# Performance work log

Hardware: AMD Instinct MI355X
Metric: run time of the kernel (lower is better)

## Reference

```python
import jax, jax.numpy as jnp
import numpy as np

B, D, ADA, INTER, RANK = 16, 2048, 1024, 1024, 8

def setup_inputs() -> dict:
    key = jax.random.key(0)
    ks = jax.random.split(key, 7)
    s = lambda fan_in: 1.0 / np.sqrt(fan_in)
    return {
        "x": jax.random.normal(ks[0], (B, D), jnp.float32),
        "ada_emb": jax.random.normal(ks[1], (B, ADA), jnp.float32),
        "base": jax.random.normal(ks[2], (D, D), jnp.float32),  # nn.Parameter(torch.randn)
        "w1": jax.random.normal(ks[3], (ADA, INTER), jnp.float32) * s(ADA),
        "b1": jax.random.normal(ks[4], (INTER,), jnp.float32) * s(ADA),
        "w2": jax.random.normal(ks[5], (INTER, D * RANK * 2), jnp.float32) * s(INTER),
        "b2": jax.random.normal(ks[6], (D * RANK * 2,), jnp.float32) * s(INTER),
    }

def reference(x, ada_emb, base, w1, b1, w2, b2):
    Bn, Dn = x.shape
    # gen_weight: Linear -> GELU (exact, erf-based as torch nn.GELU) -> Linear
    h = jax.nn.gelu(ada_emb @ w1 + b1, approximate=False)
    xw = h @ w2 + b2                               # [B, D*rank*2]
    x_a, x_b = jnp.split(xw, 2, axis=-1)
    r = x_a.shape[-1] // Dn
    x_a = x_a.reshape(Bn, Dn, r)                   # [B, D, r]
    x_b = x_b.reshape(Bn, Dn, r)                   # [B, D, r]
    # per-sample low-rank delta + base: layer[b,d,k] = base[d,k] + sum_r x_a[b,d,r]*x_b[b,k,r]
    layer = base[None, :, :] + jnp.einsum('bdr,bkr->bdk', x_a, x_b)  # [B, D, D]
    out = jnp.einsum('bc,bco->bo', x, layer)       # batched matvec
    return x + out                                 # residual
```

## Files before the change

kernel.cpp:

```cpp
#include <hip/hip_runtime.h>
#include <math.h>

#define BN 16
#define DN 2048
#define ADA 1024
#define INTER 1024
#define NW2 32768
#define HALFN 16384

__global__ void k1a(const float* __restrict__ ada, const float* __restrict__ w1,
                    float* __restrict__ h_pre) {
    const int j  = blockIdx.x * 256 + threadIdx.x;
    const int k0 = blockIdx.y * 32;
    __shared__ float a_lds[BN][32];
    for (int idx = threadIdx.x; idx < BN * 32; idx += 256) {
        int m = idx >> 5, kk = idx & 31;
        a_lds[m][kk] = ada[m * ADA + k0 + kk];
    }
    __syncthreads();
    float acc[BN];
#pragma unroll
    for (int m = 0; m < BN; ++m) acc[m] = 0.f;
    for (int kk = 0; kk < 32; ++kk) {
        float w = w1[(k0 + kk) * INTER + j];
#pragma unroll
        for (int m = 0; m < BN; ++m) acc[m] += a_lds[m][kk] * w;
    }
#pragma unroll
    for (int m = 0; m < BN; ++m) atomicAdd(&h_pre[m * INTER + j], acc[m]);
}

__global__ void k1bt(const float* __restrict__ h_pre, const float* __restrict__ b1,
                     float* __restrict__ h_t) {
    int i = blockIdx.x * 256 + threadIdx.x;
    int m = i >> 10, j = i & (INTER - 1);
    float v = h_pre[i] + b1[j];
    float g = 0.5f * v * (1.f + erff(v * 0.70710678118654752f));
    h_t[j * BN + m] = g;
}

#define K2ACC(i, hv) do { acc[i].x = fmaf((hv), w.x, acc[i].x); \
                          acc[i].y = fmaf((hv), w.y, acc[i].y); } while (0)
__global__ __launch_bounds__(256) void k2m(const float* __restrict__ h_t,
                                           const float* __restrict__ w2,
                                           float* __restrict__ p2) {
    const int n2 = blockIdx.x * 256 + threadIdx.x;
    const int k0 = blockIdx.y * 128;
    float2 acc[BN];
#pragma unroll
    for (int m = 0; m < BN; ++m) acc[m] = make_float2(0.f, 0.f);

    const float2* wp = (const float2*)w2 + (size_t)k0 * (NW2 / 2) + n2;
    const float4* hp = (const float4*)h_t + (size_t)k0 * 4;

    float2 wbuf[8];
#pragma unroll
    for (int u = 0; u < 8; ++u) wbuf[u] = wp[(size_t)u * (NW2 / 2)];

    for (int kb = 0; kb < 128; kb += 8) {
#pragma unroll
        for (int u = 0; u < 8; ++u) {
            const int k = kb + u;
            const float2 w = wbuf[u];
            const int kn = (k + 8 < 128) ? (k + 8) : k;
            wbuf[u] = wp[(size_t)kn * (NW2 / 2)];
            const float4 h0 = hp[k * 4 + 0];
            const float4 h1 = hp[k * 4 + 1];
            const float4 h2 = hp[k * 4 + 2];
            const float4 h3 = hp[k * 4 + 3];
            K2ACC(0,  h0.x); K2ACC(1,  h0.y); K2ACC(2,  h0.z); K2ACC(3,  h0.w);
            K2ACC(4,  h1.x); K2ACC(5,  h1.y); K2ACC(6,  h1.z); K2ACC(7,  h1.w);
            K2ACC(8,  h2.x); K2ACC(9,  h2.y); K2ACC(10, h2.z); K2ACC(11, h2.w);
            K2ACC(12, h3.x); K2ACC(13, h3.y); K2ACC(14, h3.z); K2ACC(15, h3.w);
        }
    }
    float2* op = (float2*)p2 + (size_t)blockIdx.y * (BN * NW2 / 2) + n2;
#pragma unroll
    for (int m = 0; m < BN; ++m) op[(size_t)m * (NW2 / 2)] = acc[m];
}

__global__ void k2r(const float* __restrict__ p2, const float* __restrict__ b2,
                    float* __restrict__ xw) {
    const int i  = blockIdx.x * 256 + threadIdx.x;
    const int n4 = i & (NW2 / 4 - 1);
    float4 s = ((const float4*)b2)[n4];
    const float4* p = (const float4*)p2 + i;
#pragma unroll
    for (int ks = 0; ks < 8; ++ks) {
        float4 v = p[(size_t)ks * (BN * NW2 / 4)];
        s.x += v.x; s.y += v.y; s.z += v.z; s.w += v.w;
    }
    ((float4*)xw)[i] = s;
}

__global__ void k3(const float* __restrict__ x, const float* __restrict__ xw,
                   float* __restrict__ t) {
    const int m = blockIdx.x >> 3, r = blockIdx.x & 7;
    float s = 0.f;
    for (int c = threadIdx.x; c < DN; c += 256)
        s += x[m * DN + c] * xw[(size_t)m * NW2 + c * 8 + r];
    __shared__ float red[256];
    red[threadIdx.x] = s;
    __syncthreads();
    for (int off = 128; off > 0; off >>= 1) {
        if (threadIdx.x < off) red[threadIdx.x] += red[threadIdx.x + off];
        __syncthreads();
    }
    if (threadIdx.x == 0) t[m * 8 + r] = red[0];
}

#define K4ACC(i, xv) do { acc[i].x = fmaf((xv), b.x, acc[i].x); \
                          acc[i].y = fmaf((xv), b.y, acc[i].y); \
                          acc[i].z = fmaf((xv), b.z, acc[i].z); \
                          acc[i].w = fmaf((xv), b.w, acc[i].w); } while (0)
__global__ __launch_bounds__(256) void k4m(const float* __restrict__ x,
                                           const float* __restrict__ base,
                                           float* __restrict__ p4) {
    const int o4 = blockIdx.x * 256 + threadIdx.x;
    const int c0 = blockIdx.y * 32;
    const int m0 = blockIdx.z * 8;
    float4 acc[8];
#pragma unroll
    for (int m = 0; m < 8; ++m) acc[m] = make_float4(0.f, 0.f, 0.f, 0.f);

    const float4* bp = (const float4*)base + (size_t)c0 * (DN / 4) + o4;
    float4 bbuf[8];
#pragma unroll
    for (int u = 0; u < 8; ++u) bbuf[u] = bp[(size_t)u * (DN / 4)];

    for (int cb = 0; cb < 32; cb += 8) {
#pragma unroll
        for (int u = 0; u < 8; ++u) {
            const int cc = cb + u;
            const float4 b = bbuf[u];
            const int cn = (cc + 8 < 32) ? (cc + 8) : cc;
            bbuf[u] = bp[(size_t)cn * (DN / 4)];
            const float x0 = x[(m0 + 0) * DN + c0 + cc];
            const float x1 = x[(m0 + 1) * DN + c0 + cc];
            const float x2 = x[(m0 + 2) * DN + c0 + cc];
            const float x3 = x[(m0 + 3) * DN + c0 + cc];
            const float x4 = x[(m0 + 4) * DN + c0 + cc];
            const float x5 = x[(m0 + 5) * DN + c0 + cc];
            const float x6 = x[(m0 + 6) * DN + c0 + cc];
            const float x7 = x[(m0 + 7) * DN + c0 + cc];
            K4ACC(0, x0); K4ACC(1, x1); K4ACC(2, x2); K4ACC(3, x3);
            K4ACC(4, x4); K4ACC(5, x5); K4ACC(6, x6); K4ACC(7, x7);
        }
    }
    float4* op = (float4*)p4 + (size_t)blockIdx.y * (BN * DN / 4)
               + (size_t)m0 * (DN / 4) + o4;
#pragma unroll
    for (int m = 0; m < 8; ++m) op[(size_t)m * (DN / 4)] = acc[m];
}

__global__ void k5(const float* __restrict__ x, const float* __restrict__ p4,
                   const float* __restrict__ xw, const float* __restrict__ t,
                   float* __restrict__ out) {
    const int i = blockIdx.x * 256 + threadIdx.x;
    const int m = i >> 11, o = i & (DN - 1);
    float s = x[i];
    const float* p = p4 + i;
#pragma unroll 8
    for (int ks = 0; ks < 64; ++ks) s += p[ks * (BN * DN)];
    const float4 xb0 = *(const float4*)(xw + (size_t)m * NW2 + HALFN + o * 8);
    const float4 xb1 = *(const float4*)(xw + (size_t)m * NW2 + HALFN + o * 8 + 4);
    const float* tm = t + m * 8;
    s += tm[0] * xb0.x + tm[1] * xb0.y + tm[2] * xb0.z + tm[3] * xb0.w
       + tm[4] * xb1.x + tm[5] * xb1.y + tm[6] * xb1.z + tm[7] * xb1.w;
    out[i] = s;
}

extern "C" void kernel_launch(void* const* d_in, const int* in_sizes, int n_in,
                              void* d_out, int out_size, void* d_ws, size_t ws_size,
                              hipStream_t stream) {
    const float* x    = (const float*)d_in[0];
    const float* ada  = (const float*)d_in[1];
    const float* base = (const float*)d_in[2];
    const float* w1   = (const float*)d_in[3];
    const float* b1   = (const float*)d_in[4];
    const float* w2   = (const float*)d_in[5];
    const float* b2   = (const float*)d_in[6];
    float* out = (float*)d_out;
    char* ws = (char*)d_ws;

    float* p2    = (float*)(ws);
    float* xw    = (float*)(ws + 16777216);
    float* p4    = (float*)(ws + 18874368);
    float* h_pre = (float*)(ws + 27262976);
    float* h_t   = (float*)(ws + 27328512);
    float* t     = (float*)(ws + 27394048);

    hipMemsetAsync(h_pre, 0, 65536, stream);

    k1a <<<dim3(4, 32),    256, 0, stream>>>(ada, w1, h_pre);
    k1bt<<<64,             256, 0, stream>>>(h_pre, b1, h_t);
    k2m <<<dim3(64, 8),    256, 0, stream>>>(h_t, w2, p2);
    k4m <<<dim3(2, 64, 2), 256, 0, stream>>>(x, base, p4);
    k2r <<<512,            256, 0, stream>>>(p2, b2, xw);
    k3  <<<128,            256, 0, stream>>>(x, xw, t);
    k5  <<<128,            256, 0, stream>>>(x, p4, xw, t, out);
}
```

Before: 71.05 us.

## Run second gen-weight GEMM on bf16 MFMA with fewer K splits

Replaces the fp32 FMA kernel for h @ w2 with a bf16 MFMA kernel. Each block converts w2 tiles to bf16 through double-buffered shared memory, and GELU writes h directly in MFMA fragment layout. The K split drops from 8 to 4, which halves the partial-sum buffer and the reduction reads. Results lose precision because h and w2 are rounded to bf16, and the kernel stays bound by reading the large fp32 w2.

```diff
diff --git a/kernel.cpp b/kernel.cpp
--- a/kernel.cpp
+++ b/kernel.cpp
@@ -7,6 +7,16 @@
 #define INTER 1024
 #define NW2 32768
 #define HALFN 16384
+
+typedef __attribute__((ext_vector_type(8))) short short8_t;
+typedef __attribute__((ext_vector_type(8))) unsigned short ushort8_t;
+typedef __attribute__((ext_vector_type(4))) float f32x4;
+
+__device__ inline unsigned short f2bf(float f) {
+    unsigned int u = __float_as_uint(f);
+    u += 0x7FFFu + ((u >> 16) & 1u);
+    return (unsigned short)(u >> 16);
+}
 
 __global__ void k1a(const float* __restrict__ ada, const float* __restrict__ w1,
                     float* __restrict__ h_pre) {
@@ -30,53 +40,77 @@
     for (int m = 0; m < BN; ++m) atomicAdd(&h_pre[m * INTER + j], acc[m]);
 }
 
-__global__ void k1bt(const float* __restrict__ h_pre, const float* __restrict__ b1,
-                     float* __restrict__ h_t) {
+__global__ void k1bf(const float* __restrict__ h_pre, const float* __restrict__ b1,
+                     unsigned short* __restrict__ h_frag) {
     int i = blockIdx.x * 256 + threadIdx.x;
-    int m = i >> 10, j = i & (INTER - 1);
-    float v = h_pre[i] + b1[j];
+    int m = i >> 10, k = i & (INTER - 1);
+    float v = h_pre[i] + b1[k];
     float g = 0.5f * v * (1.f + erff(v * 0.70710678118654752f));
-    h_t[j * BN + m] = g;
-}
-
-#define K2ACC(i, hv) do { acc[i].x = fmaf((hv), w.x, acc[i].x); \
-                          acc[i].y = fmaf((hv), w.y, acc[i].y); } while (0)
-__global__ __launch_bounds__(256) void k2m(const float* __restrict__ h_t,
-                                           const float* __restrict__ w2,
-                                           float* __restrict__ p2) {
-    const int n2 = blockIdx.x * 256 + threadIdx.x;
-    const int k0 = blockIdx.y * 128;
-    float2 acc[BN];
-#pragma unroll
-    for (int m = 0; m < BN; ++m) acc[m] = make_float2(0.f, 0.f);
-
-    const float2* wp = (const float2*)w2 + (size_t)k0 * (NW2 / 2) + n2;
-    const float4* hp = (const float4*)h_t + (size_t)k0 * 4;
-
-    float2 wbuf[8];
-#pragma unroll
-    for (int u = 0; u < 8; ++u) wbuf[u] = wp[(size_t)u * (NW2 / 2)];
-
-    for (int kb = 0; kb < 128; kb += 8) {
-#pragma unroll
-        for (int u = 0; u < 8; ++u) {
-            const int k = kb + u;
-            const float2 w = wbuf[u];
-            const int kn = (k + 8 < 128) ? (k + 8) : k;
-            wbuf[u] = wp[(size_t)kn * (NW2 / 2)];
-            const float4 h0 = hp[k * 4 + 0];
-            const float4 h1 = hp[k * 4 + 1];
-            const float4 h2 = hp[k * 4 + 2];
-            const float4 h3 = hp[k * 4 + 3];
-            K2ACC(0,  h0.x); K2ACC(1,  h0.y); K2ACC(2,  h0.z); K2ACC(3,  h0.w);
-            K2ACC(4,  h1.x); K2ACC(5,  h1.y); K2ACC(6,  h1.z); K2ACC(7,  h1.w);
-            K2ACC(8,  h2.x); K2ACC(9,  h2.y); K2ACC(10, h2.z); K2ACC(11, h2.w);
-            K2ACC(12, h3.x); K2ACC(13, h3.y); K2ACC(14, h3.z); K2ACC(15, h3.w);
-        }
-    }
-    float2* op = (float2*)p2 + (size_t)blockIdx.y * (BN * NW2 / 2) + n2;
-#pragma unroll
-    for (int m = 0; m < BN; ++m) op[(size_t)m * (NW2 / 2)] = acc[m];
+    int ck = k >> 5;
+    int l  = ((k >> 3) & 3) * 16 + m;
+    int j  = k & 7;
+    h_frag[((ck * 64 + l) << 3) + j] = f2bf(g);
+}
+
+__global__ __launch_bounds__(256) void k2mfma(const unsigned short* __restrict__ h_frag,
+                                              const float* __restrict__ w2,
+                                              float* __restrict__ p2) {
+    const int t    = threadIdx.x;
+    const int lane = t & 63;
+    const int w    = t >> 6;
+    const int n0   = blockIdx.x * 256;
+    const int kb   = blockIdx.y;
+    __shared__ __align__(16) unsigned short smem[2][256][40];
+
+    short8_t afr[8];
+#pragma unroll
+    for (int c = 0; c < 8; ++c)
+        afr[c] = *reinterpret_cast<const short8_t*>(
+            h_frag + (((kb * 8 + c) * 64 + lane) << 3));
+
+    f32x4 acc[4];
+#pragma unroll
+    for (int i = 0; i < 4; ++i) acc[i] = (f32x4){0.f, 0.f, 0.f, 0.f};
+
+    const float* wbase = w2 + (size_t)(kb * 256) * NW2 + n0 + t;
+    float wreg[32];
+#pragma unroll
+    for (int kk = 0; kk < 32; ++kk) wreg[kk] = wbase[(size_t)kk * NW2];
+
+    for (int c = 0; c < 8; ++c) {
+        const int cur = c & 1;
+        unsigned short* row = &smem[cur][t][0];
+#pragma unroll
+        for (int q = 0; q < 4; ++q) {
+            ushort8_t v;
+#pragma unroll
+            for (int e = 0; e < 8; ++e) v[e] = f2bf(wreg[q * 8 + e]);
+            *reinterpret_cast<ushort8_t*>(row + q * 8) = v;
+        }
+        if (c < 7) {
+            const float* wn = wbase + (size_t)((c + 1) * 32) * NW2;
+#pragma unroll
+            for (int kk = 0; kk < 32; ++kk) wreg[kk] = wn[(size_t)kk * NW2];
+        }
+        __syncthreads();
+#pragma unroll
+        for (int i = 0; i < 4; ++i) {
+            const short8_t b = *reinterpret_cast<const short8_t*>(
+                &smem[cur][(w * 4 + i) * 16 + (lane & 15)][(lane >> 4) * 8]);
+            acc[i] = __builtin_amdgcn_mfma_f32_16x16x32_bf16(afr[c], b, acc[i], 0, 0, 0);
+        }
+    }
+
+    float* op = p2 + (size_t)kb * (BN * NW2);
+#pragma unroll
+    for (int i = 0; i < 4; ++i) {
+        const int n = n0 + (w * 4 + i) * 16 + (lane & 15);
+#pragma unroll
+        for (int r = 0; r < 4; ++r) {
+            const int m = (lane >> 4) * 4 + r;
+            op[(size_t)m * NW2 + n] = acc[i][r];
+        }
+    }
 }
 
 __global__ void k2r(const float* __restrict__ p2, const float* __restrict__ b2,
@@ -86,7 +120,7 @@
     float4 s = ((const float4*)b2)[n4];
     const float4* p = (const float4*)p2 + i;
 #pragma unroll
-    for (int ks = 0; ks < 8; ++ks) {
+    for (int ks = 0; ks < 4; ++ks) {
         float4 v = p[(size_t)ks * (BN * NW2 / 4)];
         s.x += v.x; s.y += v.y; s.z += v.z; s.w += v.w;
     }
@@ -183,20 +217,20 @@
     float* out = (float*)d_out;
     char* ws = (char*)d_ws;
 
-    float* p2    = (float*)(ws);
-    float* xw    = (float*)(ws + 16777216);
-    float* p4    = (float*)(ws + 18874368);
-    float* h_pre = (float*)(ws + 27262976);
-    float* h_t   = (float*)(ws + 27328512);
-    float* t     = (float*)(ws + 27394048);
+    float*          p2     = (float*)(ws);
+    float*          xw     = (float*)(ws + 8388608);
+    float*          p4     = (float*)(ws + 10485760);
+    float*          h_pre  = (float*)(ws + 18874368);
+    unsigned short* h_frag = (unsigned short*)(ws + 18939904);
+    float*          t      = (float*)(ws + 18972672);
 
     hipMemsetAsync(h_pre, 0, 65536, stream);
 
-    k1a <<<dim3(4, 32),    256, 0, stream>>>(ada, w1, h_pre);
-    k1bt<<<64,             256, 0, stream>>>(h_pre, b1, h_t);
-    k2m <<<dim3(64, 8),    256, 0, stream>>>(h_t, w2, p2);
-    k4m <<<dim3(2, 64, 2), 256, 0, stream>>>(x, base, p4);
-    k2r <<<512,            256, 0, stream>>>(p2, b2, xw);
-    k3  <<<128,            256, 0, stream>>>(x, xw, t);
-    k5  <<<128,            256, 0, stream>>>(x, p4, xw, t, out);
-}
+    k1a   <<<dim3(4, 32),    256, 0, stream>>>(ada, w1, h_pre);
+    k1bf  <<<64,             256, 0, stream>>>(h_pre, b1, h_frag);
+    k2mfma<<<dim3(128, 4),   256, 0, stream>>>(h_frag, w2, p2);
+    k4m   <<<dim3(2, 64, 2), 256, 0, stream>>>(x, base, p4);
+    k2r   <<<512,            256, 0, stream>>>(p2, b2, xw);
+    k3    <<<128,            256, 0, stream>>>(x, xw, t);
+    k5    <<<128,            256, 0, stream>>>(x, p4, xw, t, out);
+}
```

After: 101.2 us. +42.4%, slower.

## Restructure w2 GEMM with float4 columns, intra-block K split and LDS reduction

Applied to the files above, without the earlier changes.

Replaces the k2m kernel with k2n, which uses 512-thread blocks. Each block splits its 128-row K chunk across four thread groups of 32 rows each, and every thread loads float4 columns of w2. The h activations are staged in LDS, and the four partial sums are reduced through shared memory before a single coalesced write to the per-K-split partial buffer. This aims to widen the w2 loads and improve latency hiding. In exchange it raises register pressure (16 float4 accumulators), uses 32KB of LDS for the reduction, and adds serialized barriers.

```diff
diff --git a/kernel.cpp b/kernel.cpp
--- a/kernel.cpp
+++ b/kernel.cpp
@@ -39,44 +39,79 @@
     h_t[j * BN + m] = g;
 }
 
-#define K2ACC(i, hv) do { acc[i].x = fmaf((hv), w.x, acc[i].x); \
-                          acc[i].y = fmaf((hv), w.y, acc[i].y); } while (0)
-__global__ __launch_bounds__(256) void k2m(const float* __restrict__ h_t,
-                                           const float* __restrict__ w2,
-                                           float* __restrict__ p2) {
-    const int n2 = blockIdx.x * 256 + threadIdx.x;
-    const int k0 = blockIdx.y * 128;
-    float2 acc[BN];
-#pragma unroll
-    for (int m = 0; m < BN; ++m) acc[m] = make_float2(0.f, 0.f);
-
-    const float2* wp = (const float2*)w2 + (size_t)k0 * (NW2 / 2) + n2;
-    const float4* hp = (const float4*)h_t + (size_t)k0 * 4;
-
-    float2 wbuf[8];
-#pragma unroll
-    for (int u = 0; u < 8; ++u) wbuf[u] = wp[(size_t)u * (NW2 / 2)];
-
-    for (int kb = 0; kb < 128; kb += 8) {
+__global__ __launch_bounds__(512, 4) void k2n(const float* __restrict__ h_t,
+                                              const float* __restrict__ w2,
+                                              float* __restrict__ p2) {
+    const int tid  = threadIdx.x;
+    const int ksub = tid >> 7;
+    const int tn   = tid & 127;
+    const int kb0  = blockIdx.y * 128;
+    const int k0   = kb0 + ksub * 32;
+
+    __shared__ float hl[128][16];
+    __shared__ float red[16][512];
+
+    ((float4*)hl)[tid] = ((const float4*)(h_t + kb0 * BN))[tid];
+    __syncthreads();
+
+    float4 acc[BN];
+#pragma unroll
+    for (int m = 0; m < BN; ++m) acc[m] = make_float4(0.f, 0.f, 0.f, 0.f);
+
+    const float4* wp = (const float4*)w2 + (size_t)k0 * (NW2 / 4)
+                     + blockIdx.x * 128 + tn;
+    float4 wbuf[8];
+#pragma unroll
+    for (int u = 0; u < 8; ++u) wbuf[u] = wp[(size_t)u * (NW2 / 4)];
+
+    for (int ko = 0; ko < 4; ++ko) {
 #pragma unroll
         for (int u = 0; u < 8; ++u) {
-            const int k = kb + u;
-            const float2 w = wbuf[u];
-            const int kn = (k + 8 < 128) ? (k + 8) : k;
-            wbuf[u] = wp[(size_t)kn * (NW2 / 2)];
-            const float4 h0 = hp[k * 4 + 0];
-            const float4 h1 = hp[k * 4 + 1];
-            const float4 h2 = hp[k * 4 + 2];
-            const float4 h3 = hp[k * 4 + 3];
-            K2ACC(0,  h0.x); K2ACC(1,  h0.y); K2ACC(2,  h0.z); K2ACC(3,  h0.w);
-            K2ACC(4,  h1.x); K2ACC(5,  h1.y); K2ACC(6,  h1.z); K2ACC(7,  h1.w);
-            K2ACC(8,  h2.x); K2ACC(9,  h2.y); K2ACC(10, h2.z); K2ACC(11, h2.w);
-            K2ACC(12, h3.x); K2ACC(13, h3.y); K2ACC(14, h3.z); K2ACC(15, h3.w);
+            const int kk = ko * 8 + u;
+            const float4 wv = wbuf[u];
+            const int nk = (kk + 8 < 32) ? kk + 8 : kk;
+            wbuf[u] = wp[(size_t)nk * (NW2 / 4)];
+            const float* hk = &hl[ksub * 32 + kk][0];
+            const float4 h0 = *(const float4*)(hk + 0);
+            const float4 h1 = *(const float4*)(hk + 4);
+            const float4 h2 = *(const float4*)(hk + 8);
+            const float4 h3 = *(const float4*)(hk + 12);
+#define A2(m, hs) do { acc[m].x = fmaf(hs, wv.x, acc[m].x); \
+                       acc[m].y = fmaf(hs, wv.y, acc[m].y); \
+                       acc[m].z = fmaf(hs, wv.z, acc[m].z); \
+                       acc[m].w = fmaf(hs, wv.w, acc[m].w); } while (0)
+            A2(0, h0.x);  A2(1, h0.y);  A2(2, h0.z);  A2(3, h0.w);
+            A2(4, h1.x);  A2(5, h1.y);  A2(6, h1.z);  A2(7, h1.w);
+            A2(8, h2.x);  A2(9, h2.y);  A2(10, h2.z); A2(11, h2.w);
+            A2(12, h3.x); A2(13, h3.y); A2(14, h3.z); A2(15, h3.w);
+#undef A2
         }
     }
-    float2* op = (float2*)p2 + (size_t)blockIdx.y * (BN * NW2 / 2) + n2;
-#pragma unroll
-    for (int m = 0; m < BN; ++m) op[(size_t)m * (NW2 / 2)] = acc[m];
+
+    if (ksub == 0) {
+#pragma unroll
+        for (int m = 0; m < BN; ++m) *(float4*)&red[m][tn * 4] = acc[m];
+    }
+    __syncthreads();
+#pragma unroll
+    for (int s = 1; s < 4; ++s) {
+        if (ksub == s) {
+#pragma unroll
+            for (int m = 0; m < BN; ++m) {
+                float4 r = *(float4*)&red[m][tn * 4];
+                r.x += acc[m].x; r.y += acc[m].y; r.z += acc[m].z; r.w += acc[m].w;
+                *(float4*)&red[m][tn * 4] = r;
+            }
+        }
+        __syncthreads();
+    }
+
+    float* op = p2 + (size_t)blockIdx.y * (BN * NW2) + blockIdx.x * 512 + tn * 4;
+#pragma unroll
+    for (int q = 0; q < 4; ++q) {
+        const int m = ksub + q * 4;
+        *(float4*)(op + (size_t)m * NW2) = *(float4*)&red[m][tn * 4];
+    }
 }
 
 __global__ void k2r(const float* __restrict__ p2, const float* __restrict__ b2,
@@ -194,7 +229,7 @@
 
     k1a <<<dim3(4, 32),    256, 0, stream>>>(ada, w1, h_pre);
     k1bt<<<64,             256, 0, stream>>>(h_pre, b1, h_t);
-    k2m <<<dim3(64, 8),    256, 0, stream>>>(h_t, w2, p2);
+    k2n <<<dim3(64, 8),    512, 0, stream>>>(h_t, w2, p2);
     k4m <<<dim3(2, 64, 2), 256, 0, stream>>>(x, base, p4);
     k2r <<<512,            256, 0, stream>>>(p2, b2, xw);
     k3  <<<128,            256, 0, stream>>>(x, xw, t);
```

Measured after the change: 108.9 us. 53.4% more time.

## Stage w2 tiles through LDS with async global_load_lds double buffering

Applied to the files above, without the earlier changes.

Replaces the register-prefetch k2m GEMM with k2g, which streams w2 tiles into a double-buffered LDS area using the global_load_lds builtin while computing the previous tile. Each thread now produces float4 outputs across 16 batch rows. The split-K factor goes from 8 to 16 with smaller K slices, so twice as many partial sums are written and reduced in k2r. This aims to overlap the dominant w2 memory stream with compute and raise parallelism, at the cost of a larger partial-sum buffer and more reduction traffic.

```diff
diff --git a/kernel.cpp b/kernel.cpp
--- a/kernel.cpp
+++ b/kernel.cpp
@@ -7,6 +7,13 @@
 #define INTER 1024
 #define NW2 32768
 #define HALFN 16384
+#define KSL 16
+
+typedef __attribute__((address_space(1))) const void gv_t;
+typedef __attribute__((address_space(3))) void lv_t;
+__device__ __forceinline__ void gload_lds16(const float* g, float* l) {
+    __builtin_amdgcn_global_load_lds((gv_t*)g, (lv_t*)l, 16, 0, 0);
+}
 
 __global__ void k1a(const float* __restrict__ ada, const float* __restrict__ w1,
                     float* __restrict__ h_pre) {
@@ -39,44 +46,67 @@
     h_t[j * BN + m] = g;
 }
 
-#define K2ACC(i, hv) do { acc[i].x = fmaf((hv), w.x, acc[i].x); \
-                          acc[i].y = fmaf((hv), w.y, acc[i].y); } while (0)
-__global__ __launch_bounds__(256) void k2m(const float* __restrict__ h_t,
+__global__ __launch_bounds__(256) void k2g(const float* __restrict__ h_t,
                                            const float* __restrict__ w2,
                                            float* __restrict__ p2) {
-    const int n2 = blockIdx.x * 256 + threadIdx.x;
-    const int k0 = blockIdx.y * 128;
-    float2 acc[BN];
-#pragma unroll
-    for (int m = 0; m < BN; ++m) acc[m] = make_float2(0.f, 0.f);
-
-    const float2* wp = (const float2*)w2 + (size_t)k0 * (NW2 / 2) + n2;
-    const float4* hp = (const float4*)h_t + (size_t)k0 * 4;
-
-    float2 wbuf[8];
-#pragma unroll
-    for (int u = 0; u < 8; ++u) wbuf[u] = wp[(size_t)u * (NW2 / 2)];
-
-    for (int kb = 0; kb < 128; kb += 8) {
-#pragma unroll
-        for (int u = 0; u < 8; ++u) {
-            const int k = kb + u;
-            const float2 w = wbuf[u];
-            const int kn = (k + 8 < 128) ? (k + 8) : k;
-            wbuf[u] = wp[(size_t)kn * (NW2 / 2)];
-            const float4 h0 = hp[k * 4 + 0];
-            const float4 h1 = hp[k * 4 + 1];
-            const float4 h2 = hp[k * 4 + 2];
-            const float4 h3 = hp[k * 4 + 3];
-            K2ACC(0,  h0.x); K2ACC(1,  h0.y); K2ACC(2,  h0.z); K2ACC(3,  h0.w);
-            K2ACC(4,  h1.x); K2ACC(5,  h1.y); K2ACC(6,  h1.z); K2ACC(7,  h1.w);
-            K2ACC(8,  h2.x); K2ACC(9,  h2.y); K2ACC(10, h2.z); K2ACC(11, h2.w);
-            K2ACC(12, h3.x); K2ACC(13, h3.y); K2ACC(14, h3.z); K2ACC(15, h3.w);
-        }
-    }
-    float2* op = (float2*)p2 + (size_t)blockIdx.y * (BN * NW2 / 2) + n2;
-#pragma unroll
-    for (int m = 0; m < BN; ++m) op[(size_t)m * (NW2 / 2)] = acc[m];
+    const int tid = threadIdx.x;
+    const int wv_ = tid >> 6, ln_ = tid & 63;
+    const int n0  = blockIdx.x * 1024;
+    const int k0  = blockIdx.y * 64;
+    __shared__ __align__(16) float wl[2][8][1024];
+    __shared__ __align__(16) float hl[64][16];
+
+    ((float4*)hl)[tid] = ((const float4*)(h_t + k0 * BN))[tid];
+
+    float4 acc[BN];
+#pragma unroll
+    for (int m = 0; m < BN; ++m) acc[m] = make_float4(0.f, 0.f, 0.f, 0.f);
+
+#define STAGE(buf, ph) do {                                                   \
+    const float* gs_ = w2 + (size_t)(k0 + (ph) * 8) * NW2 + n0                \
+                     + wv_ * 256 + ln_ * 4;                                   \
+    float* ls_ = &wl[buf][0][wv_ * 256];                                      \
+    _Pragma("unroll")                                                         \
+    for (int i_ = 0; i_ < 8; ++i_)                                            \
+        gload_lds16(gs_ + (size_t)i_ * NW2, ls_ + i_ * 1024);                 \
+} while (0)
+
+#define COMPUTE(buf, ph) do {                                                 \
+    _Pragma("unroll")                                                         \
+    for (int i_ = 0; i_ < 8; ++i_) {                                          \
+        const int kk_ = (ph) * 8 + i_;                                        \
+        const float4 wvv = ((const float4*)wl[buf][i_])[tid];                 \
+        const float4 h0 = ((const float4*)&hl[kk_][0])[0];                    \
+        const float4 h1 = ((const float4*)&hl[kk_][0])[1];                    \
+        const float4 h2 = ((const float4*)&hl[kk_][0])[2];                    \
+        const float4 h3 = ((const float4*)&hl[kk_][0])[3];                    \
+        AC(0,  h0.x); AC(1,  h0.y); AC(2,  h0.z); AC(3,  h0.w);               \
+        AC(4,  h1.x); AC(5,  h1.y); AC(6,  h1.z); AC(7,  h1.w);               \
+        AC(8,  h2.x); AC(9,  h2.y); AC(10, h2.z); AC(11, h2.w);               \
+        AC(12, h3.x); AC(13, h3.y); AC(14, h3.z); AC(15, h3.w);               \
+    }                                                                         \
+} while (0)
+#define AC(m, hs) do { acc[m].x = fmaf(hs, wvv.x, acc[m].x);                  \
+                       acc[m].y = fmaf(hs, wvv.y, acc[m].y);                  \
+                       acc[m].z = fmaf(hs, wvv.z, acc[m].z);                  \
+                       acc[m].w = fmaf(hs, wvv.w, acc[m].w); } while (0)
+
+    STAGE(0, 0);
+    __syncthreads();
+    for (int ph = 0; ph < 8; ++ph) {
+        const int cur = ph & 1;
+        if (ph < 7) STAGE(cur ^ 1, ph + 1);
+        COMPUTE(cur, ph);
+        __syncthreads();
+    }
+#undef AC
+#undef COMPUTE
+#undef STAGE
+
+    float* op = p2 + (size_t)blockIdx.y * (BN * NW2) + n0 + tid * 4;
+#pragma unroll
+    for (int m = 0; m < BN; ++m)
+        *(float4*)(op + (size_t)m * NW2) = acc[m];
 }
 
 __global__ void k2r(const float* __restrict__ p2, const float* __restrict__ b2,
@@ -86,7 +116,7 @@
     float4 s = ((const float4*)b2)[n4];
     const float4* p = (const float4*)p2 + i;
 #pragma unroll
-    for (int ks = 0; ks < 8; ++ks) {
+    for (int ks = 0; ks < KSL; ++ks) {
         float4 v = p[(size_t)ks * (BN * NW2 / 4)];
         s.x += v.x; s.y += v.y; s.z += v.z; s.w += v.w;
     }
@@ -184,17 +214,17 @@
     char* ws = (char*)d_ws;
 
     float* p2    = (float*)(ws);
-    float* xw    = (float*)(ws + 16777216);
-    float* p4    = (float*)(ws + 18874368);
-    float* h_pre = (float*)(ws + 27262976);
-    float* h_t   = (float*)(ws + 27328512);
-    float* t     = (float*)(ws + 27394048);
+    float* xw    = (float*)(ws + 33554432);
+    float* p4    = (float*)(ws + 35651584);
+    float* h_pre = (float*)(ws + 44040192);
+    float* h_t   = (float*)(ws + 44105728);
+    float* t     = (float*)(ws + 44171264);
 
     hipMemsetAsync(h_pre, 0, 65536, stream);
 
     k1a <<<dim3(4, 32),    256, 0, stream>>>(ada, w1, h_pre);
     k1bt<<<64,             256, 0, stream>>>(h_pre, b1, h_t);
-    k2m <<<dim3(64, 8),    256, 0, stream>>>(h_t, w2, p2);
+    k2g <<<dim3(32, KSL),  256, 0, stream>>>(h_t, w2, p2);
     k4m <<<dim3(2, 64, 2), 256, 0, stream>>>(x, base, p4);
     k2r <<<512,            256, 0, stream>>>(p2, b2, xw);
     k3  <<<128,            256, 0, stream>>>(x, xw, t);
```

New measurement: 82.32 us. +15.9%, slower.
